# Performance work log

Hardware: AMD Instinct MI355X
Metric: run time of the kernel (lower is better)

The kernel has to match this reference:

```python
import jax, jax.numpy as jnp
import numpy as np
from jax import lax

B, CIN, L, COUT, K = 64, 64, 4096, 128, 7
STRIDE, PAD = 1, 3
POOL, POOL_STRIDE = 2, 2
BN_EPS = 1e-5


def setup_inputs() -> dict:
    key = jax.random.key(0)
    ks = jax.random.split(key, 7)
    I = jax.random.normal(ks[0], (B, CIN, L), jnp.float32)
    bn_gamma = 1.0 + 0.1 * jax.random.normal(ks[1], (CIN,), jnp.float32)
    bn_beta = 0.1 * jax.random.normal(ks[2], (CIN,), jnp.float32)
    bn_mean = 0.1 * jax.random.normal(ks[3], (CIN,), jnp.float32)
    bn_var = jax.random.uniform(ks[4], (CIN,), jnp.float32, 0.5, 1.5)
    conv_w = 0.05 * jax.random.normal(ks[5], (COUT, CIN, K), jnp.float32)
    # XNOR-Net style per-output-channel scale alpha = mean(|W|) over (Cin, K)
    alpha = jnp.mean(jnp.abs(conv_w), axis=(1, 2))  # [COUT]
    prelu_w = jnp.full((1,), 0.25, jnp.float32)  # nn.PReLU() default: 1 shared param
    return dict(I=I, bn_gamma=bn_gamma, bn_beta=bn_beta, bn_mean=bn_mean,
                bn_var=bn_var, conv_w=conv_w, alpha=alpha, prelu_w=prelu_w)


def reference(I, bn_gamma, bn_beta, bn_mean, bn_var, conv_w, alpha, prelu_w):
    # BatchNorm1d (eval mode: running stats), per-channel over dim 1
    scale = (bn_gamma / jnp.sqrt(bn_var + BN_EPS))[None, :, None]
    x = (I - bn_mean[None, :, None]) * scale + bn_beta[None, :, None]
    # Binarize (sign; sign(0)=0 matches torch.sign)
    x = jnp.sign(x)
    # Conv1d, no bias, zero padding=3, stride=1  -> [B, COUT, L]
    y = lax.conv_general_dilated(x, conv_w, window_strides=(STRIDE,),
                                 padding=[(PAD, PAD)],
                                 dimension_numbers=('NCH', 'OIH', 'NCH'))
    # alpha scale (per output channel)
    y = y * alpha[None, :, None]
    # PReLU with single shared parameter
    y = jnp.where(y > 0, y, prelu_w[0] * y)
    # MaxPool1d(kernel=2, stride=2)
    y = lax.reduce_window(y, -jnp.inf, lax.max,
                          (1, 1, POOL), (1, 1, POOL_STRIDE), 'VALID')
    return y
```

## Files before the change

### kernel.cpp

```cpp
#include <hip/hip_runtime.h>
#include <hip/hip_bf16.h>
#include <stdint.h>

#define BATCH 64
#define CIN   64
#define LEN   4096
#define COUT  128
#define KW    7
#define LPOOL 2048
#define NT    4
#define RROWS 72
#define RAWP  80
#define SPITCH 64

typedef __bf16 v8bf __attribute__((ext_vector_type(8)));
typedef unsigned short v8us __attribute__((ext_vector_type(8)));
typedef float  v4f  __attribute__((ext_vector_type(4)));

typedef const __attribute__((address_space(1))) void* gp1_t;
typedef __attribute__((address_space(3))) void* lp3_t;

__global__ __launch_bounds__(256)
void wconv_kernel(const float* __restrict__ W, ushort* __restrict__ Wt) {
    int i = blockIdx.x * 256 + threadIdx.x;
    if (i >= COUT * CIN * KW) return;
    int co  = i / (CIN * KW);
    int rem = i - co * (CIN * KW);
    int ci  = rem / KW;
    int k   = rem - ci * KW;
    uint u = __float_as_uint(W[i]);
    uint r = (u + 0x7FFFu + ((u >> 16) & 1u)) >> 16;
    Wt[(k * COUT + co) * CIN + ci] = (ushort)r;
}

static __device__ __forceinline__ void sync_lds() {
    asm volatile("s_waitcnt lgkmcnt(0)" ::: "memory");
    __builtin_amdgcn_s_barrier();
}
static __device__ __forceinline__ void wait_vm0() {
    asm volatile("s_waitcnt vmcnt(0)" ::: "memory");
}

__global__ __launch_bounds__(256, 3)
void conv_kernel(const float* __restrict__ I,
                 const float* __restrict__ bn_g, const float* __restrict__ bn_b,
                 const float* __restrict__ bn_m, const float* __restrict__ bn_v,
                 const ushort* __restrict__ Wt,
                 const float* __restrict__ alpha, const float* __restrict__ prelu,
                 float* __restrict__ out) {
    __shared__ __attribute__((aligned(16))) float  raw[CIN * RAWP];
    __shared__ __attribute__((aligned(16))) ushort stg[2][RROWS * SPITCH];

    int tid = threadIdx.x;
    int lane = tid & 63, wave = tid >> 6;
    int b = blockIdx.y, bx = blockIdx.x;
    int l0base = bx * (64 * NT);

    const float* Ib = I + (size_t)b * CIN * LEN;

    float* rawb = raw + wave * 1280;
    const char* gb[5]; int cb[5];
    #pragma unroll
    for (int i = 0; i < 5; ++i) {
        int m = i * 64 + lane;
        int cil = m / 20;
        int c   = m - 20 * cil;
        cb[i] = 16 * c - 32;
        gb[i] = (const char*)(Ib + (size_t)(16 * wave + cil) * LEN) + cb[i];
    }

    auto dma_tile = [&](int l0t) {
        int l4 = 4 * l0t;
        #pragma unroll
        for (int i = 0; i < 5; ++i) {
            int off = cb[i] + l4;
            if (off >= 0 && off + 16 <= LEN * 4)
                __builtin_amdgcn_global_load_lds((gp1_t)(gb[i] + l4),
                                                 (lp3_t)(rawb + i * 256), 16, 0, 0);
        }
    };

    dma_tile(l0base);

    int oc  = lane & 1;
    int brq = lane >> 1;
    int g8  = 2 * wave + oc;
    float sc[8], mn[8], bt[8];
    if (lane < 36) {
        #pragma unroll
        for (int c = 0; c < 8; ++c) {
            int ci = 8 * g8 + c;
            sc[c] = __fdiv_rn(bn_g[ci], __fsqrt_rn(__fadd_rn(bn_v[ci], 1e-5f)));
            mn[c] = bn_m[ci];
            bt[c] = bn_b[ci];
        }
    }

    int quad = lane >> 4, lr = lane & 15;
    int cout0 = wave * 32;
    const ushort* wbase = Wt + ((size_t)cout0 + lr) * CIN + quad * 8;
    float pw  = prelu[0];
    float al0 = alpha[cout0 + lr];
    float al1 = alpha[cout0 + 16 + lr];
    float* obase = out + ((size_t)b * COUT) * LPOOL + bx * (32 * NT);

    v8bf c00 = *(const v8bf*)(wbase);
    v8bf c01 = *(const v8bf*)(wbase + 16 * CIN);
    v8bf c10 = *(const v8bf*)(wbase + 32);
    v8bf c11 = *(const v8bf*)(wbase + 32 + 16 * CIN);

    auto binarize = [&](int l0t, int buf) {
        if (lane < 36) {
            const float4* r4 = (const float4*)rawb;
            float4 fr[8];
            #pragma unroll
            for (int c = 0; c < 8; ++c)
                fr[c] = r4[(8 * oc + c) * 20 + brq + 1];
            ushort* sb = &stg[buf][0];
            #pragma unroll
            for (int j = 0; j < 4; ++j) {
                int r = 4 * brq + j;
                int p = l0t - 4 + r;
                bool pok = (p >= 0) && (p < LEN);
                v8us u;
                #pragma unroll
                for (int c = 0; c < 8; ++c) {
                    float v = ((const float*)&fr[c])[j];
                    float x = __fadd_rn(__fmul_rn(__fsub_rn(v, mn[c]), sc[c]), bt[c]);
                    ushort s = x > 0.f ? (ushort)0x3F80 : (x < 0.f ? (ushort)0xBF80 : (ushort)0);
                    u[c] = pok ? s : (ushort)0;
                }
                *(v8us*)(&sb[r * SPITCH + ((g8 ^ (r & 7)) << 3)]) = u;
            }
        }
    };

    wait_vm0();
    binarize(l0base, 0);
    if (NT > 1) dma_tile(l0base + 64);
    sync_lds();

    for (int t = 0; t < NT; ++t) {
        int l0 = l0base + t * 64;
        const ushort* sb_cur = &stg[t & 1][0];

        v4f acc[4][2];
        #pragma unroll
        for (int mt = 0; mt < 4; ++mt) { acc[mt][0] = (v4f)0.f; acc[mt][1] = (v4f)0.f; }

        #pragma unroll 1
        for (int k = 0; k < KW; ++k) {
            int nk = (k == KW - 1) ? 0 : k + 1;
            const ushort* wn = wbase + nk * COUT * CIN;
            v8bf n00 = *(const v8bf*)(wn);
            v8bf n01 = *(const v8bf*)(wn + 16 * CIN);
            v8bf n10 = *(const v8bf*)(wn + 32);
            v8bf n11 = *(const v8bf*)(wn + 32 + 16 * CIN);

            int rk = lr + 1 + k;
            int s8 = rk & 7;
            const ushort* a0p = &sb_cur[rk * SPITCH + ((quad ^ s8) << 3)];
            const ushort* a1p = &sb_cur[rk * SPITCH + (((quad ^ 4) ^ s8) << 3)];
            #pragma unroll
            for (int mt = 0; mt < 4; ++mt) {
                v8bf a0 = *(const v8bf*)(a0p + mt * 16 * SPITCH);
                v8bf a1 = *(const v8bf*)(a1p + mt * 16 * SPITCH);
                acc[mt][0] = __builtin_amdgcn_mfma_f32_16x16x32_bf16(a0, c00, acc[mt][0], 0, 0, 0);
                acc[mt][1] = __builtin_amdgcn_mfma_f32_16x16x32_bf16(a0, c01, acc[mt][1], 0, 0, 0);
                acc[mt][0] = __builtin_amdgcn_mfma_f32_16x16x32_bf16(a1, c10, acc[mt][0], 0, 0, 0);
                acc[mt][1] = __builtin_amdgcn_mfma_f32_16x16x32_bf16(a1, c11, acc[mt][1], 0, 0, 0);
            }
            c00 = n00; c01 = n01; c10 = n10; c11 = n11;
        }

        float pv[2][4][2];
        #pragma unroll
        for (int n2 = 0; n2 < 2; ++n2) {
            float al = n2 ? al1 : al0;
            #pragma unroll
            for (int mt = 0; mt < 4; ++mt) {
                float v0 = acc[mt][n2][0] * al; v0 = v0 > 0.f ? v0 : pw * v0;
                float v1 = acc[mt][n2][1] * al; v1 = v1 > 0.f ? v1 : pw * v1;
                float v2 = acc[mt][n2][2] * al; v2 = v2 > 0.f ? v2 : pw * v2;
                float v3 = acc[mt][n2][3] * al; v3 = v3 > 0.f ? v3 : pw * v3;
                pv[n2][mt][0] = fmaxf(v0, v1);
                pv[n2][mt][1] = fmaxf(v2, v3);
            }
        }

        if (t + 1 < NT) {
            wait_vm0();
            binarize(l0 + 64, (t + 1) & 1);
        }
        if (t + 2 < NT) dma_tile(l0 + 128);

        float* ob = obase + t * 32;
        #pragma unroll
        for (int n2 = 0; n2 < 2; ++n2) {
            int co = cout0 + n2 * 16 + lr;
            float* ocp = ob + (size_t)co * LPOOL + quad * 2;
            #pragma unroll
            for (int mt = 0; mt < 4; ++mt)
                *(float2*)(ocp + mt * 8) = make_float2(pv[n2][mt][0], pv[n2][mt][1]);
        }

        sync_lds();
    }
}

extern "C" void kernel_launch(void* const* d_in, const int* in_sizes, int n_in,
                              void* d_out, int out_size, void* d_ws, size_t ws_size,
                              hipStream_t stream) {
    const float* I      = (const float*)d_in[0];
    const float* bn_g   = (const float*)d_in[1];
    const float* bn_b   = (const float*)d_in[2];
    const float* bn_m   = (const float*)d_in[3];
    const float* bn_v   = (const float*)d_in[4];
    const float* conv_w = (const float*)d_in[5];
    const float* alpha  = (const float*)d_in[6];
    const float* prelu  = (const float*)d_in[7];
    float* out = (float*)d_out;

    ushort* Wt = (ushort*)d_ws;

    wconv_kernel<<<(COUT * CIN * KW + 255) / 256, 256, 0, stream>>>(conv_w, Wt);
    dim3 grid(LEN / (64 * NT), BATCH);
    conv_kernel<<<grid, 256, 0, stream>>>(I, bn_g, bn_b, bn_m, bn_v, Wt, alpha, prelu, out);
}
```

Measured before the change: 191.4 us.

## Keep all conv weights resident in registers and double tiles per block

Loads all seven kernel taps' bf16 weight fragments into registers once per block instead of reloading per tap from global memory inside the loop. The tap loop is fully unrolled with scheduling barriers. Each block also processes twice as many length tiles, which amortises the weight load and prologue. This raises register pressure (launch bounds lowered to 2 blocks/SM) and halves the grid, which lowers occupancy and parallelism.

```diff
diff --git a/kernel.cpp b/kernel.cpp
--- a/kernel.cpp
+++ b/kernel.cpp
@@ -8,7 +8,7 @@
 #define COUT  128
 #define KW    7
 #define LPOOL 2048
-#define NT    4
+#define NT    8
 #define RROWS 72
 #define RAWP  80
 #define SPITCH 64
@@ -41,7 +41,7 @@
     asm volatile("s_waitcnt vmcnt(0)" ::: "memory");
 }
 
-__global__ __launch_bounds__(256, 3)
+__global__ __launch_bounds__(256, 2)
 void conv_kernel(const float* __restrict__ I,
                  const float* __restrict__ bn_g, const float* __restrict__ bn_b,
                  const float* __restrict__ bn_m, const float* __restrict__ bn_v,
@@ -104,10 +104,15 @@
     float al1 = alpha[cout0 + 16 + lr];
     float* obase = out + ((size_t)b * COUT) * LPOOL + bx * (32 * NT);
 
-    v8bf c00 = *(const v8bf*)(wbase);
-    v8bf c01 = *(const v8bf*)(wbase + 16 * CIN);
-    v8bf c10 = *(const v8bf*)(wbase + 32);
-    v8bf c11 = *(const v8bf*)(wbase + 32 + 16 * CIN);
+    v8bf wreg[KW][2][2];
+    #pragma unroll
+    for (int k = 0; k < KW; ++k) {
+        const ushort* wk = wbase + (size_t)k * COUT * CIN;
+        wreg[k][0][0] = *(const v8bf*)(wk);
+        wreg[k][0][1] = *(const v8bf*)(wk + 16 * CIN);
+        wreg[k][1][0] = *(const v8bf*)(wk + 32);
+        wreg[k][1][1] = *(const v8bf*)(wk + 32 + 16 * CIN);
+    }
 
     auto binarize = [&](int l0t, int buf) {
         if (lane < 36) {
@@ -137,7 +142,7 @@
 
     wait_vm0();
     binarize(l0base, 0);
-    if (NT > 1) dma_tile(l0base + 64);
+    dma_tile(l0base + 64);
     sync_lds();
 
     for (int t = 0; t < NT; ++t) {
@@ -148,15 +153,8 @@
         #pragma unroll
         for (int mt = 0; mt < 4; ++mt) { acc[mt][0] = (v4f)0.f; acc[mt][1] = (v4f)0.f; }
 
-        #pragma unroll 1
+        #pragma unroll
         for (int k = 0; k < KW; ++k) {
-            int nk = (k == KW - 1) ? 0 : k + 1;
-            const ushort* wn = wbase + nk * COUT * CIN;
-            v8bf n00 = *(const v8bf*)(wn);
-            v8bf n01 = *(const v8bf*)(wn + 16 * CIN);
-            v8bf n10 = *(const v8bf*)(wn + 32);
-            v8bf n11 = *(const v8bf*)(wn + 32 + 16 * CIN);
-
             int rk = lr + 1 + k;
             int s8 = rk & 7;
             const ushort* a0p = &sb_cur[rk * SPITCH + ((quad ^ s8) << 3)];
@@ -165,12 +163,12 @@
             for (int mt = 0; mt < 4; ++mt) {
                 v8bf a0 = *(const v8bf*)(a0p + mt * 16 * SPITCH);
                 v8bf a1 = *(const v8bf*)(a1p + mt * 16 * SPITCH);
-                acc[mt][0] = __builtin_amdgcn_mfma_f32_16x16x32_bf16(a0, c00, acc[mt][0], 0, 0, 0);
-                acc[mt][1] = __builtin_amdgcn_mfma_f32_16x16x32_bf16(a0, c01, acc[mt][1], 0, 0, 0);
-                acc[mt][0] = __builtin_amdgcn_mfma_f32_16x16x32_bf16(a1, c10, acc[mt][0], 0, 0, 0);
-                acc[mt][1] = __builtin_amdgcn_mfma_f32_16x16x32_bf16(a1, c11, acc[mt][1], 0, 0, 0);
+                acc[mt][0] = __builtin_amdgcn_mfma_f32_16x16x32_bf16(a0, wreg[k][0][0], acc[mt][0], 0, 0, 0);
+                acc[mt][1] = __builtin_amdgcn_mfma_f32_16x16x32_bf16(a0, wreg[k][0][1], acc[mt][1], 0, 0, 0);
+                acc[mt][0] = __builtin_amdgcn_mfma_f32_16x16x32_bf16(a1, wreg[k][1][0], acc[mt][0], 0, 0, 0);
+                acc[mt][1] = __builtin_amdgcn_mfma_f32_16x16x32_bf16(a1, wreg[k][1][1], acc[mt][1], 0, 0, 0);
             }
-            c00 = n00; c01 = n01; c10 = n10; c11 = n11;
+            __builtin_amdgcn_sched_barrier(0);
         }
 
         float pv[2][4][2];
```

Result: faster. 167.5 us (-12.5%).
